# Optimization experiments

Hardware: AMD Instinct MI355X
Metric: run time of the kernel (lower is better)

Reference implementation:

```python
import jax, jax.numpy as jnp
import numpy as np

N, E, D, H, K = 8192, 8, 1024, 4096, 2


def setup_inputs() -> dict:
    key = jax.random.key(0)
    ks = jax.random.split(key, 12)
    s = 0.02  # init scale for weights
    return {
        "x": jax.random.normal(ks[0], (N, D), jnp.float32),
        "noise": jax.random.normal(ks[1], (N, E), jnp.float32),
        "Wg_w": jax.random.normal(ks[2], (D, E), jnp.float32) * s,
        "Wg_b": jnp.zeros((E,), jnp.float32),
        "Wn_w": jax.random.normal(ks[3], (D, E), jnp.float32) * s,
        "Wn_b": jnp.zeros((E,), jnp.float32),
        "w1": jax.random.normal(ks[4], (E, D, H), jnp.float32) * s,
        "b1": jnp.zeros((E, H), jnp.float32),
        "w2": jax.random.normal(ks[5], (E, H, D), jnp.float32) * s,
        "b2": jnp.zeros((E, D), jnp.float32),
        "k": K,
    }


def reference(x, noise, Wg_w, Wg_b, Wn_w, Wn_b, w1, b1, w2, b2, k):
    # --- noisy top-k gating: H(x) = Wg(x) + noise * softplus(Wn(x)) ---
    g_logits = x @ Wg_w + Wg_b                       # [N, E]
    n_scale = jax.nn.softplus(x @ Wn_w + Wn_b)       # [N, E]
    h = g_logits + noise * n_scale                   # [N, E]
    topk_vals, topk_inds = jax.lax.top_k(h, k)       # [N, k]
    gates = jax.nn.softmax(topk_vals, axis=-1)       # [N, k]

    # Scatter top-k gates into a dense [N, E] map (zeros for unselected experts),
    # so the weighted combine is exactly sum_j gates[n,j] * expert_{inds[n,j]}(x_n).
    n_tok, n_exp = h.shape
    dense_gates = jnp.zeros((n_tok, n_exp), h.dtype).at[
        jnp.arange(n_tok)[:, None], topk_inds
    ].set(gates)                                     # [N, E]

    # --- per-expert 2-layer MLP: fc2(relu(fc1(x))) ---
    hid = jax.nn.relu(jnp.einsum('nd,edh->neh', x, w1) + b1)  # [N, E, H]
    y = jnp.einsum('neh,ehd->ned', hid, w2) + b2              # [N, E, D]
    out = jnp.einsum('ned,ne->nd', y, dense_gates)            # [N, D]
    return out
```

## Files before the change

### kernel.cpp

```cpp
#include <hip/hip_runtime.h>
#include <hip/hip_bf16.h>

#define NTOK 8192
#define NEXP 8
#define DMODEL 1024
#define DHID 4096

typedef __bf16 bf16x8 __attribute__((ext_vector_type(8)));
typedef float f32x4 __attribute__((ext_vector_type(4)));

__device__ __forceinline__ unsigned short f2bf(float f) {
  return __builtin_bit_cast(unsigned short, __float2bfloat16(f));
}

__device__ __forceinline__ void gload_lds16(const void* g, void* l) {
  __builtin_amdgcn_global_load_lds(
      (const __attribute__((address_space(1))) unsigned int*)g,
      (__attribute__((address_space(3))) unsigned int*)l, 16, 0, 0);
}

__device__ __forceinline__ int imin(int a, int b) { return a < b ? a : b; }

constexpr size_t OFF_XB   = 0;
constexpr size_t OFF_W1T  = OFF_XB + (size_t)NTOK * DMODEL * 2;
constexpr size_t OFF_W2T  = OFF_W1T + (size_t)NEXP * DHID * DMODEL * 2;
constexpr size_t OFF_HID  = OFF_W2T + (size_t)NEXP * DMODEL * DHID * 2;
constexpr size_t OFF_IDX  = OFF_HID + (size_t)NTOK * 2 * DHID * 2;
constexpr size_t OFF_GATE = OFF_IDX + (size_t)NTOK * 2 * 4;
constexpr size_t OFF_LIST = OFF_GATE + (size_t)NTOK * 2 * 4;
constexpr size_t OFF_CNT  = OFF_LIST + (size_t)NTOK * 2 * 4;
constexpr size_t OFF_OFFS = OFF_CNT + 128;
constexpr size_t OFF_CUR  = OFF_OFFS + 128;

__global__ void transpose_bf16_kernel(const float* __restrict__ in,
                                      unsigned short* __restrict__ out,
                                      int R, int C) {
  __shared__ float sh[64][65];
  const size_t ebase = (size_t)blockIdx.z * R * C;
  const float* ine = in + ebase;
  unsigned short* oute = out + ebase;
  int c0 = blockIdx.x * 64, r0 = blockIdx.y * 64;
  int tx = threadIdx.x & 15, ty = threadIdx.x >> 4;
#pragma unroll
  for (int p = 0; p < 4; ++p) {
    int row = ty + p * 16;
    float4 v = *(const float4*)&ine[(size_t)(r0 + row) * C + c0 + tx * 4];
    sh[row][tx * 4 + 0] = v.x;
    sh[row][tx * 4 + 1] = v.y;
    sh[row][tx * 4 + 2] = v.z;
    sh[row][tx * 4 + 3] = v.w;
  }
  __syncthreads();
#pragma unroll
  for (int p = 0; p < 4; ++p) {
    int crow = ty + p * 16;
    ushort4 o;
    o.x = f2bf(sh[tx * 4 + 0][crow]);
    o.y = f2bf(sh[tx * 4 + 1][crow]);
    o.z = f2bf(sh[tx * 4 + 2][crow]);
    o.w = f2bf(sh[tx * 4 + 3][crow]);
    *(ushort4*)&oute[(size_t)(c0 + crow) * R + r0 + tx * 4] = o;
  }
}

__global__ void gating_kernel(const float* __restrict__ x,
                              const float* __restrict__ noise,
                              const float* __restrict__ Wg_w,
                              const float* __restrict__ Wg_b,
                              const float* __restrict__ Wn_w,
                              const float* __restrict__ Wn_b,
                              unsigned short* __restrict__ xb,
                              int* __restrict__ topk_idx,
                              float* __restrict__ topk_gate,
                              int* __restrict__ counts) {
  int wave = threadIdx.x >> 6;
  int lane = threadIdx.x & 63;
  int n = blockIdx.x * 4 + wave;
  if (n >= NTOK) return;

  float ag[8] = {0.f, 0.f, 0.f, 0.f, 0.f, 0.f, 0.f, 0.f};
  float an[8] = {0.f, 0.f, 0.f, 0.f, 0.f, 0.f, 0.f, 0.f};
  const float* xr = x + (size_t)n * DMODEL;
  unsigned short* xbr = xb + (size_t)n * DMODEL;
#pragma unroll 4
  for (int i = 0; i < DMODEL / 64; ++i) {
    int d = lane + i * 64;
    float xv = xr[d];
    xbr[d] = f2bf(xv);
    const float4* wg = (const float4*)(Wg_w + (size_t)d * 8);
    const float4* wn = (const float4*)(Wn_w + (size_t)d * 8);
    float4 g0 = wg[0], g1 = wg[1];
    float4 n0 = wn[0], n1 = wn[1];
    ag[0] += xv * g0.x; ag[1] += xv * g0.y; ag[2] += xv * g0.z; ag[3] += xv * g0.w;
    ag[4] += xv * g1.x; ag[5] += xv * g1.y; ag[6] += xv * g1.z; ag[7] += xv * g1.w;
    an[0] += xv * n0.x; an[1] += xv * n0.y; an[2] += xv * n0.z; an[3] += xv * n0.w;
    an[4] += xv * n1.x; an[5] += xv * n1.y; an[6] += xv * n1.z; an[7] += xv * n1.w;
  }
#pragma unroll
  for (int off = 32; off > 0; off >>= 1) {
#pragma unroll
    for (int j = 0; j < 8; ++j) {
      ag[j] += __shfl_down(ag[j], off, 64);
      an[j] += __shfl_down(an[j], off, 64);
    }
  }
  if (lane == 0) {
    float h[8];
#pragma unroll
    for (int e = 0; e < 8; ++e) {
      float gl = ag[e] + Wg_b[e];
      float z = an[e] + Wn_b[e];
      float sp = fmaxf(z, 0.f) + log1pf(expf(-fabsf(z)));
      h[e] = gl + noise[(size_t)n * 8 + e] * sp;
    }
    int i0 = 0; float v0 = h[0];
#pragma unroll
    for (int e = 1; e < 8; ++e)
      if (h[e] > v0) { v0 = h[e]; i0 = e; }
    int i1 = -1; float v1 = -1e30f;
#pragma unroll
    for (int e = 0; e < 8; ++e)
      if (e != i0 && h[e] > v1) { v1 = h[e]; i1 = e; }
    float e1 = expf(v1 - v0);
    float inv = 1.f / (1.f + e1);
    topk_idx[n * 2] = i0;
    topk_idx[n * 2 + 1] = i1;
    topk_gate[n * 2] = inv;
    topk_gate[n * 2 + 1] = e1 * inv;
    atomicAdd(&counts[i0], 1);
    atomicAdd(&counts[i1], 1);
  }
}

__global__ void scan_kernel(const int* __restrict__ counts,
                            int* __restrict__ offsets, int* __restrict__ cursor) {
  if (threadIdx.x == 0) {
    int acc = 0;
    for (int e = 0; e < NEXP; ++e) {
      offsets[e] = acc;
      cursor[e] = acc;
      acc += counts[e];
    }
    offsets[NEXP] = acc;
  }
}

__global__ void scatter_kernel(const int* __restrict__ topk_idx,
                               int* __restrict__ cursor, int* __restrict__ list) {
  int n = blockIdx.x * 256 + threadIdx.x;
  if (n >= NTOK) return;
#pragma unroll
  for (int j = 0; j < 2; ++j) {
    int e = topk_idx[n * 2 + j];
    int pos = atomicAdd(&cursor[e], 1);
    list[pos] = n * 2 + j;
  }
}

template <int MODE>
__global__ __launch_bounds__(256) void expert_gemm(
    const unsigned short* __restrict__ Asrc, const unsigned short* __restrict__ Bt,
    const float* __restrict__ bias, const int* __restrict__ offsets,
    const int* __restrict__ list, const float* __restrict__ gates,
    unsigned short* __restrict__ hid, float* __restrict__ out) {
  constexpr int K = MODE ? DHID : DMODEL;
  constexpr int Nout = MODE ? DMODEL : DHID;
  constexpr int NT = K / 32;

  const int gx = gridDim.x;
  const int lin = blockIdx.x + gx * (blockIdx.y + 64 * blockIdx.z);
  const int e = lin & 7;
  const int r = lin >> 3;
  const int by = r & 63;
  const int bx = r >> 6;

  const int off = offsets[e];
  const int ne = offsets[e + 1] - off;
  const int m0 = by * 128;
  if (m0 >= ne) return;
  const int n0 = bx * 128;

  __shared__ alignas(16) unsigned short Al[2][128 * 32];
  __shared__ alignas(16) unsigned short Bl[2][128 * 32];

  const int tid = threadIdx.x;
  const int lane = tid & 63;
  const int w = tid >> 6;
  const int wm = (w >> 1) * 64;
  const int wn = (w & 1) * 64;
  const int lr = lane & 15;
  const int kg = lane >> 4;
  const int chrd = ((kg ^ (lr & 3)) * 8);

  const unsigned short* srcA[2];
  const unsigned short* srcB[2];
#pragma unroll
  for (int i = 0; i < 2; ++i) {
    int q = tid + i * 256;
    int rr = q >> 2, c = q & 3;
    int cs = c ^ (rr & 3);
    int p = off + imin(m0 + rr, ne - 1);
    if (MODE == 0) {
      int token = list[p] >> 1;
      srcA[i] = Asrc + (size_t)token * DMODEL + cs * 8;
    } else {
      srcA[i] = Asrc + (size_t)p * DHID + cs * 8;
    }
    srcB[i] = Bt + (size_t)e * Nout * K + (size_t)(n0 + rr) * K + cs * 8;
  }

  f32x4 acc[4][4] = {};

  auto stage = [&](int buf, int kt) {
#pragma unroll
    for (int i = 0; i < 2; ++i) {
      int q = tid + i * 256;
      gload_lds16(srcA[i] + kt * 32, &Al[buf][q * 8]);
      gload_lds16(srcB[i] + kt * 32, &Bl[buf][q * 8]);
    }
  };

  auto compute = [&](int buf) {
    bf16x8 af[4], bfr[4];
#pragma unroll
    for (int mf = 0; mf < 4; ++mf)
      af[mf] = *(const bf16x8*)&Al[buf][(wm + mf * 16 + lr) * 32 + chrd];
#pragma unroll
    for (int nf = 0; nf < 4; ++nf)
      bfr[nf] = *(const bf16x8*)&Bl[buf][(wn + nf * 16 + lr) * 32 + chrd];
#pragma unroll
    for (int mf = 0; mf < 4; ++mf)
#pragma unroll
      for (int nf = 0; nf < 4; ++nf)
        acc[mf][nf] = __builtin_amdgcn_mfma_f32_16x16x32_bf16(af[mf], bfr[nf],
                                                              acc[mf][nf], 0, 0, 0);
  };

  stage(0, 0);
  __syncthreads();
  int cur = 0;
  for (int t = 0; t < NT; ++t) {
    if (t + 1 < NT) stage(cur ^ 1, t + 1);
    compute(cur);
    __syncthreads();
    cur ^= 1;
  }

  if (MODE == 0) {
#pragma unroll
    for (int mf = 0; mf < 4; ++mf) {
#pragma unroll
      for (int j = 0; j < 4; ++j) {
        int rloc = wm + mf * 16 + kg * 4 + j;
        int row = m0 + rloc;
        if (row < ne) {
          size_t p = (size_t)(off + row);
#pragma unroll
          for (int nf = 0; nf < 4; ++nf) {
            int col = n0 + wn + nf * 16 + lr;
            float v = acc[mf][nf][j] + bias[(size_t)e * Nout + col];
            hid[p * DHID + col] = f2bf(fmaxf(v, 0.f));
          }
        }
      }
    }
  } else {
#pragma unroll
    for (int mf = 0; mf < 4; ++mf) {
#pragma unroll
      for (int j = 0; j < 4; ++j) {
        int rloc = wm + mf * 16 + kg * 4 + j;
        int row = m0 + rloc;
        if (row < ne) {
          int lv = list[off + row];
          int token = lv >> 1;
          float g = gates[lv];
#pragma unroll
          for (int nf = 0; nf < 4; ++nf) {
            int col = n0 + wn + nf * 16 + lr;
            float v = (acc[mf][nf][j] + bias[(size_t)e * Nout + col]) * g;
            atomicAdd(&out[(size_t)token * DMODEL + col], v);
          }
        }
      }
    }
  }
}

extern "C" void kernel_launch(void* const* d_in, const int* in_sizes, int n_in,
                              void* d_out, int out_size, void* d_ws, size_t ws_size,
                              hipStream_t stream) {
  const float* x = (const float*)d_in[0];
  const float* noise = (const float*)d_in[1];
  const float* Wg_w = (const float*)d_in[2];
  const float* Wg_b = (const float*)d_in[3];
  const float* Wn_w = (const float*)d_in[4];
  const float* Wn_b = (const float*)d_in[5];
  const float* w1 = (const float*)d_in[6];
  const float* b1 = (const float*)d_in[7];
  const float* w2 = (const float*)d_in[8];
  const float* b2 = (const float*)d_in[9];
  float* out = (float*)d_out;

  char* ws = (char*)d_ws;
  unsigned short* xb = (unsigned short*)(ws + OFF_XB);
  unsigned short* w1t = (unsigned short*)(ws + OFF_W1T);
  unsigned short* w2t = (unsigned short*)(ws + OFF_W2T);
  unsigned short* hid = (unsigned short*)(ws + OFF_HID);
  int* topk_idx = (int*)(ws + OFF_IDX);
  float* topk_gate = (float*)(ws + OFF_GATE);
  int* list = (int*)(ws + OFF_LIST);
  int* counts = (int*)(ws + OFF_CNT);
  int* offsets = (int*)(ws + OFF_OFFS);
  int* cursor = (int*)(ws + OFF_CUR);

  hipMemsetAsync(out, 0, (size_t)NTOK * DMODEL * sizeof(float), stream);
  hipMemsetAsync(counts, 0, NEXP * sizeof(int), stream);

  transpose_bf16_kernel<<<dim3(DHID / 64, DMODEL / 64, NEXP), 256, 0, stream>>>(
      w1, w1t, DMODEL, DHID);
  transpose_bf16_kernel<<<dim3(DMODEL / 64, DHID / 64, NEXP), 256, 0, stream>>>(
      w2, w2t, DHID, DMODEL);

  gating_kernel<<<NTOK / 4, 256, 0, stream>>>(x, noise, Wg_w, Wg_b, Wn_w, Wn_b,
                                              xb, topk_idx, topk_gate, counts);
  scan_kernel<<<1, 64, 0, stream>>>(counts, offsets, cursor);
  scatter_kernel<<<NTOK / 256, 256, 0, stream>>>(topk_idx, cursor, list);

  expert_gemm<0><<<dim3(DHID / 128, 64, NEXP), 256, 0, stream>>>(
      xb, w1t, b1, offsets, list, topk_gate, hid, nullptr);
  expert_gemm<1><<<dim3(DMODEL / 128, 64, NEXP), 256, 0, stream>>>(
      hid, w2t, b2, offsets, list, topk_gate, nullptr, out);
}
```

Measured before the change: 913.9 us.

## Triple-buffer expert GEMM LDS with explicit vmcnt waits and new swizzle

Moves the expert GEMM from a double-buffered to a triple-buffered LDS pipeline that prefetches two k-tiles ahead. Each tile uses explicit s_waitcnt vmcnt counts and raw s_barrier in place of __syncthreads, so more global loads stay in flight while MFMAs run. The LDS swizzle changes from lr&3 to (lr>>1)&3 to reduce bank conflicts. LDS use grows by half, which may lower occupancy, and the hand-counted waits must match the number of loads issued per stage.

After: 864.6 us. -5.4%, faster.

```diff
diff --git a/kernel.cpp b/kernel.cpp
--- a/kernel.cpp
+++ b/kernel.cpp
@@ -157,6 +157,8 @@
   }
 }
 
+#define VMW(N) asm volatile("s_waitcnt vmcnt(" #N ")" ::: "memory")
+
 template <int MODE>
 __global__ __launch_bounds__(256) void expert_gemm(
     const unsigned short* __restrict__ Asrc, const unsigned short* __restrict__ Bt,
@@ -180,8 +182,8 @@
   if (m0 >= ne) return;
   const int n0 = bx * 128;
 
-  __shared__ alignas(16) unsigned short Al[2][128 * 32];
-  __shared__ alignas(16) unsigned short Bl[2][128 * 32];
+  __shared__ alignas(16) unsigned short Al[3][128 * 32];
+  __shared__ alignas(16) unsigned short Bl[3][128 * 32];
 
   const int tid = threadIdx.x;
   const int lane = tid & 63;
@@ -190,7 +192,7 @@
   const int wn = (w & 1) * 64;
   const int lr = lane & 15;
   const int kg = lane >> 4;
-  const int chrd = ((kg ^ (lr & 3)) * 8);
+  const int chrd = (kg ^ ((lr >> 1) & 3)) * 8;
 
   const unsigned short* srcA[2];
   const unsigned short* srcB[2];
@@ -198,7 +200,7 @@
   for (int i = 0; i < 2; ++i) {
     int q = tid + i * 256;
     int rr = q >> 2, c = q & 3;
-    int cs = c ^ (rr & 3);
+    int cs = c ^ ((rr >> 1) & 3);
     int p = off + imin(m0 + rr, ne - 1);
     if (MODE == 0) {
       int token = list[p] >> 1;
@@ -211,23 +213,25 @@
 
   f32x4 acc[4][4] = {};
 
-  auto stage = [&](int buf, int kt) {
+  auto stage = [&](int slot, int kt) {
 #pragma unroll
     for (int i = 0; i < 2; ++i) {
       int q = tid + i * 256;
-      gload_lds16(srcA[i] + kt * 32, &Al[buf][q * 8]);
-      gload_lds16(srcB[i] + kt * 32, &Bl[buf][q * 8]);
+      gload_lds16(srcA[i] + kt * 32, &Al[slot][q * 8]);
+      gload_lds16(srcB[i] + kt * 32, &Bl[slot][q * 8]);
     }
   };
 
-  auto compute = [&](int buf) {
+  auto compute = [&](int slot) {
     bf16x8 af[4], bfr[4];
 #pragma unroll
     for (int mf = 0; mf < 4; ++mf)
-      af[mf] = *(const bf16x8*)&Al[buf][(wm + mf * 16 + lr) * 32 + chrd];
+      af[mf] = *(const bf16x8*)&Al[slot][(wm + mf * 16 + lr) * 32 + chrd];
 #pragma unroll
     for (int nf = 0; nf < 4; ++nf)
-      bfr[nf] = *(const bf16x8*)&Bl[buf][(wn + nf * 16 + lr) * 32 + chrd];
+      bfr[nf] = *(const bf16x8*)&Bl[slot][(wn + nf * 16 + lr) * 32 + chrd];
+    asm volatile("s_waitcnt lgkmcnt(0)" ::: "memory");
+    __builtin_amdgcn_sched_barrier(0);
 #pragma unroll
     for (int mf = 0; mf < 4; ++mf)
 #pragma unroll
@@ -237,13 +241,22 @@
   };
 
   stage(0, 0);
-  __syncthreads();
+  stage(1, 1);
+  stage(2, 2);
+
   int cur = 0;
   for (int t = 0; t < NT; ++t) {
-    if (t + 1 < NT) stage(cur ^ 1, t + 1);
+    if (t < NT - 2) { VMW(8); }
+    else if (t == NT - 2) { VMW(4); }
+    else { VMW(0); }
+    __builtin_amdgcn_s_barrier();
+    __builtin_amdgcn_sched_barrier(0);
     compute(cur);
-    __syncthreads();
-    cur ^= 1;
+    asm volatile("s_waitcnt lgkmcnt(0)" ::: "memory");
+    __builtin_amdgcn_sched_barrier(0);
+    __builtin_amdgcn_s_barrier();
+    if (t + 3 < NT) stage(cur, t + 3);
+    cur = (cur == 2) ? 0 : cur + 1;
   }
 
   if (MODE == 0) {
```
